# Kernel tuning notes

Measured on AMD Instinct MI355X. Metric: run time of the kernel, lower is better.

Reference implementation:

```python
import jax, jax.numpy as jnp
import numpy as np

N = 100000   # nodes
E = 1600000  # edges (avg degree 16)
F = 128      # num_features
H = 128      # hidden_channels
L = 3        # mp_layers
C = 40       # num_classes
EPS = 1e-5   # BatchNorm eps


def setup_inputs() -> dict:
    key = jax.random.key(0)
    ks = jax.random.split(key, 6)
    x = jax.random.normal(ks[0], (N, F), dtype=jnp.float32)
    edge_index = jax.random.randint(ks[1], (2, E), 0, N, dtype=jnp.int64)
    # GCNConv weights (F==H so all layers share shape), PyG-style lin + bias
    Ws = jax.random.normal(ks[2], (L, H, H), dtype=jnp.float32) * 0.05
    bs = jnp.zeros((L, H), dtype=jnp.float32)
    # BatchNorm affine params
    gammas = jnp.ones((L, H), dtype=jnp.float32)
    betas = jnp.zeros((L, H), dtype=jnp.float32)
    # output head: skip-concat dim = F + L*H
    W_out = jax.random.normal(ks[3], (F + L * H, C), dtype=jnp.float32) * 0.05
    b_out = jnp.zeros((C,), dtype=jnp.float32)
    return {"x": x, "Ws": Ws, "bs": bs, "gammas": gammas, "betas": betas,
            "W_out": W_out, "b_out": b_out, "edge_index": edge_index}


def reference(x, Ws, bs, gammas, betas, W_out, b_out, edge_index):
    src, dst = edge_index[0], edge_index[1]
    n = x.shape[0]
    # GCN symmetric normalization with self-loops (PyG gcn_norm, add_self_loops=True)
    deg = jax.ops.segment_sum(jnp.ones(src.shape[0], x.dtype), dst, num_segments=n) + 1.0
    dinv = jax.lax.rsqrt(deg)
    edge_norm = (dinv[src] * dinv[dst])[:, None]   # [E,1]
    self_norm = (dinv * dinv)[:, None]             # [N,1] self-loop contribution

    outs = [x]
    h = x
    for i in range(L):
        hw = h @ Ws[i]                                                   # [N,H]
        msg = hw[src] * edge_norm                                        # gather [E,H]
        agg = jax.ops.segment_sum(msg, dst, num_segments=n)              # scatter-add
        agg = agg + hw * self_norm + bs[i]
        # BatchNorm1d in training mode (batch stats, biased variance)
        mu = agg.mean(axis=0)
        var = agg.var(axis=0)
        h = gammas[i] * (agg - mu) * jax.lax.rsqrt(var + EPS) + betas[i]
        outs.append(h)  # dropout p=0.0 -> identity; skip=True collects each layer

    xcat = jnp.concatenate(outs, axis=1)  # [N, F + L*H]
    return xcat @ W_out + b_out
```

## Files before the change

kernel.cpp:

```cpp
#include <hip/hip_runtime.h>

#define NN 100000
#define NE 1600000
#define HD 128
#define NL 3
#define NC 40
#define NCP 48

#define NBK 196
#define NPB 512
#define BSH 9
#define CAP 9216
#define PCAP 13312
#define EPB 6400
#define NBINBLK 250

typedef unsigned int u32;
typedef unsigned short u16;
typedef __attribute__((ext_vector_type(8))) short short8;
typedef __attribute__((ext_vector_type(4))) float f32x4;

__device__ __forceinline__ float b2f(u16 h){
    union{u32 u; float f;} v; v.u = ((u32)h) << 16; return v.f;
}
__device__ __forceinline__ u16 f2b(float f){
    union{float f; u32 u;} v; v.f = f;
    u32 u = v.u;
    u32 r = (u + 0x7FFFu + ((u >> 16) & 1u)) >> 16;
    return (u16)r;
}

__global__ void k_conv_w(const float* __restrict__ Ws, u16* __restrict__ wt,
                         int* __restrict__ gcur, float* __restrict__ stats,
                         u16* __restrict__ hwzero, const float* __restrict__ Wout,
                         u16* __restrict__ woutt){
    int i = blockIdx.x * blockDim.x + threadIdx.x;
    if (i < NBK) gcur[i] = 0;
    if (i < NL * 2 * HD) stats[i] = 0.f;
    if (i < HD) hwzero[i] = 0;
    if (i < NL * NCP * HD){
        int l = i / (NCP * HD);
        int r = i % (NCP * HD);
        int n = r / HD;
        int k = r % HD;
        woutt[i] = (n < NC) ? f2b(Wout[(size_t)(HD + l * HD + k) * NC + n]) : (u16)0;
    }
    if (i >= NL * HD * HD) return;
    int l = i / (HD * HD);
    int r = i % (HD * HD);
    int n = r / HD;
    int k = r % HD;
    wt[i] = f2b(Ws[l * HD * HD + k * HD + n]);
}

__launch_bounds__(256)
__global__ void k_convhead(const float* __restrict__ x, const float* __restrict__ wout,
                           const float* __restrict__ bout, float* __restrict__ out,
                           u16* __restrict__ hA){
    __shared__ float wl[HD * NC];
    __shared__ float bl[NC];
    int tid = threadIdx.x;
    for (int i = tid; i < HD * NC; i += 256) wl[i] = wout[i];
    if (tid < NC) bl[tid] = bout[tid];
    __syncthreads();
    int n = blockIdx.x * 256 + tid;
    if (n >= NN) return;
    f32x4 acc[10];
    #pragma unroll
    for (int q = 0; q < 10; q++) acc[q] = *reinterpret_cast<const f32x4*>(&bl[q * 4]);
    const float* xr = x + (size_t)n * HD;
    #pragma unroll
    for (int k8 = 0; k8 < HD / 8; k8++){
        float4 v0 = reinterpret_cast<const float4*>(xr)[k8 * 2];
        float4 v1 = reinterpret_cast<const float4*>(xr)[k8 * 2 + 1];
        float xs[8] = {v0.x, v0.y, v0.z, v0.w, v1.x, v1.y, v1.z, v1.w};
        uint4 ov;
        u16* po = (u16*)&ov;
        #pragma unroll
        for (int t = 0; t < 8; t++){
            int f = k8 * 8 + t;
            po[t] = f2b(xs[t]);
            const f32x4* wr = reinterpret_cast<const f32x4*>(&wl[f * NC]);
            #pragma unroll
            for (int q = 0; q < 10; q++) acc[q] += xs[t] * wr[q];
        }
        reinterpret_cast<uint4*>(hA + (size_t)n * HD)[k8] = ov;
    }
    float* orw = out + (size_t)n * NC;
    #pragma unroll
    for (int q = 0; q < 10; q++) reinterpret_cast<f32x4*>(orw)[q] = acc[q];
}

__launch_bounds__(256)
__global__ void k_bin(const int* __restrict__ src, const int* __restrict__ dst,
                      int* __restrict__ gcur, uint2* __restrict__ bb){
    __shared__ int hist[NBK];
    __shared__ int lbase[NBK];
    __shared__ int gbase[NBK];
    __shared__ int cur[NBK];
    __shared__ int wsum[4];
    __shared__ uint2 stage[EPB];
    int tid = threadIdx.x;
    int e0 = blockIdx.x * EPB;
    for (int i = tid; i < NBK; i += 256) hist[i] = 0;
    __syncthreads();
    for (int k = tid; k < EPB; k += 256){
        int d = dst[e0 + k];
        atomicAdd(&hist[d >> BSH], 1);
    }
    __syncthreads();
    {
        int v = (tid < NBK) ? hist[tid] : 0;
        int lane = tid & 63, w = tid >> 6;
        int incl = v;
        #pragma unroll
        for (int dlt = 1; dlt < 64; dlt <<= 1){
            int t = __shfl_up(incl, dlt);
            if (lane >= dlt) incl += t;
        }
        if (lane == 63) wsum[w] = incl;
        __syncthreads();
        if (tid == 0){
            int run = 0;
            #pragma unroll
            for (int j = 0; j < 4; j++){ int t = wsum[j]; wsum[j] = run; run += t; }
        }
        __syncthreads();
        int excl = wsum[w] + incl - v;
        if (tid < NBK){ lbase[tid] = excl; cur[tid] = excl; }
    }
    __syncthreads();
    if (tid < NBK) gbase[tid] = atomicAdd(&gcur[tid], hist[tid]);
    __syncthreads();
    for (int k = tid; k < EPB; k += 256){
        int s = src[e0 + k], d = dst[e0 + k];
        int pos = atomicAdd(&cur[d >> BSH], 1);
        stage[pos] = make_uint2((u32)s, (u32)d);
    }
    __syncthreads();
    for (int k = tid; k < EPB; k += 256){
        uint2 sd = stage[k];
        int b = (int)(sd.y >> BSH);
        int g = gbase[b] + (k - lbase[b]);
        if (g < CAP) bb[(size_t)b * CAP + g] = sd;
    }
}

__launch_bounds__(512)
__global__ void k_csr(const int* __restrict__ gcur, const uint2* __restrict__ bb,
                      int* __restrict__ csr_src, int* __restrict__ offs,
                      int* __restrict__ oend, float* __restrict__ dinv){
    __shared__ int hist[NPB];
    __shared__ int cur[NPB];
    __shared__ int wsum[8];
    __shared__ int totp_s;
    __shared__ int lcsr[PCAP];
    int tid = threadIdx.x;
    int b = blockIdx.x;
    int cnt_b = gcur[b]; if (cnt_b > CAP) cnt_b = CAP;
    const uint2* eb = bb + (size_t)b * CAP;
    hist[tid] = 0;
    __syncthreads();
    for (int k = tid; k < cnt_b; k += 512)
        atomicAdd(&hist[eb[k].y & (NPB - 1)], 1);
    __syncthreads();
    int cnt = hist[tid];
    int ps = (1 + cnt + 7) & ~7;
    int lane = tid & 63, w = tid >> 6;
    int incl = ps;
    #pragma unroll
    for (int dlt = 1; dlt < 64; dlt <<= 1){
        int t = __shfl_up(incl, dlt);
        if (lane >= dlt) incl += t;
    }
    if (lane == 63) wsum[w] = incl;
    __syncthreads();
    if (tid == 0){
        int run = 0;
        #pragma unroll
        for (int j = 0; j < 8; j++){ int t = wsum[j]; wsum[j] = run; run += t; }
        totp_s = run;
    }
    __syncthreads();
    int excl = wsum[w] + incl - ps;
    int n = b * NPB + tid;
    offs[n] = b * PCAP + excl;
    oend[n] = b * PCAP + excl + ps;
    if (n < NN) dinv[n] = rsqrtf((float)(cnt + 1));
    cur[tid] = excl + 1;
    int totp = totp_s;
    __syncthreads();
    for (int k = tid; k < totp; k += 512) lcsr[k] = NN;
    __syncthreads();
    lcsr[excl] = (n < NN) ? n : NN;
    __syncthreads();
    for (int k = tid; k < cnt_b; k += 512){
        uint2 sd = eb[k];
        int pos = atomicAdd(&cur[sd.y & (NPB - 1)], 1);
        lcsr[pos] = (int)sd.x;
    }
    __syncthreads();
    for (int k = tid; k < totp; k += 512)
        csr_src[b * PCAP + k] = lcsr[k];
}

__launch_bounds__(256)
__global__ void k_gemm(const u16* __restrict__ h, const u16* __restrict__ wt,
                       const float* __restrict__ dinv, u16* __restrict__ out){
    __shared__ u16 wlds[HD * HD];
    int tid = threadIdx.x;
    {
        const uint4* g = reinterpret_cast<const uint4*>(wt);
        #pragma unroll
        for (int i = 0; i < 8; i++){
            int lin16 = tid + 256 * i;
            uint4 v = g[lin16];
            int c = lin16 >> 4;
            int addr16 = lin16 ^ (c & 7);
            reinterpret_cast<uint4*>(wlds)[addr16] = v;
        }
    }
    __syncthreads();

    int wv = tid >> 6, lane = tid & 63;
    int row_base = blockIdx.x * 64 + wv * 16;
    int arow = row_base + (lane & 15);
    if (arow >= NN) arow = NN - 1;
    int koff = (lane >> 4) * 8;

    f32x4 acc[8];
    #pragma unroll
    for (int t = 0; t < 8; t++) acc[t] = (f32x4){0.f, 0.f, 0.f, 0.f};

    #pragma unroll
    for (int kk = 0; kk < 4; kk++){
        short8 a = *reinterpret_cast<const short8*>(h + arow * HD + kk * 32 + koff);
        #pragma unroll
        for (int ct = 0; ct < 8; ct++){
            int c = ct * 16 + (lane & 15);
            int addr16 = (c * 16 + kk * 4 + (koff >> 3)) ^ (c & 7);
            short8 b = *reinterpret_cast<const short8*>(wlds + addr16 * 8);
            acc[ct] = __builtin_amdgcn_mfma_f32_16x16x32_bf16(a, b, acc[ct], 0, 0, 0);
        }
    }

    int drow = row_base + (lane >> 4) * 4;
    int dcol = lane & 15;
    float dv[4];
    #pragma unroll
    for (int r = 0; r < 4; r++){
        int rr = drow + r;
        dv[r] = dinv[rr < NN ? rr : NN - 1];
    }
    #pragma unroll
    for (int ct = 0; ct < 8; ct++){
        #pragma unroll
        for (int r = 0; r < 4; r++){
            int rr = drow + r;
            if (rr < NN) out[rr * HD + ct * 16 + dcol] = f2b(acc[ct][r] * dv[r]);
        }
    }
}

template<bool DO_HW>
__launch_bounds__(256)
__global__ void k_gemmbn(const u16* __restrict__ agg, const float* __restrict__ bn,
                         const u16* __restrict__ wt, const u16* __restrict__ woutt,
                         const float* __restrict__ dinv, u16* __restrict__ hw,
                         float* __restrict__ out){
    __shared__ u16 wlds[HD * HD];
    __shared__ u16 wolds[NCP * HD];
    __shared__ float Al[HD];
    __shared__ float Cl[HD];
    int tid = threadIdx.x;
    if (DO_HW){
        const uint4* g = reinterpret_cast<const uint4*>(wt);
        #pragma unroll
        for (int i = 0; i < 8; i++){
            int lin16 = tid + 256 * i;
            uint4 v = g[lin16];
            int c = lin16 >> 4;
            int addr16 = lin16 ^ (c & 7);
            reinterpret_cast<uint4*>(wlds)[addr16] = v;
        }
    }
    {
        const uint4* g = reinterpret_cast<const uint4*>(woutt);
        #pragma unroll
        for (int i = 0; i < 3; i++){
            int lin16 = tid + 256 * i;
            uint4 v = g[lin16];
            int c = lin16 >> 4;
            int addr16 = lin16 ^ (c & 7);
            reinterpret_cast<uint4*>(wolds)[addr16] = v;
        }
    }
    if (tid < HD){ Al[tid] = bn[tid]; Cl[tid] = bn[HD + tid]; }
    __syncthreads();

    int wv = tid >> 6, lane = tid & 63;
    int row_base = blockIdx.x * 64 + wv * 16;
    int arow = row_base + (lane & 15);
    if (arow >= NN) arow = NN - 1;
    int koff = (lane >> 4) * 8;

    f32x4 accW[8];
    f32x4 accH[3];
    #pragma unroll
    for (int t = 0; t < 8; t++) accW[t] = (f32x4){0.f, 0.f, 0.f, 0.f};
    #pragma unroll
    for (int t = 0; t < 3; t++) accH[t] = (f32x4){0.f, 0.f, 0.f, 0.f};

    #pragma unroll
    for (int kk = 0; kk < 4; kk++){
        int fb = kk * 32 + koff;
        short8 raw = *reinterpret_cast<const short8*>(agg + (size_t)arow * HD + fb);
        f32x4 A0 = *reinterpret_cast<const f32x4*>(&Al[fb]);
        f32x4 A1 = *reinterpret_cast<const f32x4*>(&Al[fb + 4]);
        f32x4 C0 = *reinterpret_cast<const f32x4*>(&Cl[fb]);
        f32x4 C1 = *reinterpret_cast<const f32x4*>(&Cl[fb + 4]);
        short8 a;
        #pragma unroll
        for (int j = 0; j < 4; j++){
            a[j]     = (short)f2b(b2f((u16)raw[j])     * A0[j] + C0[j]);
            a[j + 4] = (short)f2b(b2f((u16)raw[j + 4]) * A1[j] + C1[j]);
        }
        if (DO_HW){
            #pragma unroll
            for (int ct = 0; ct < 8; ct++){
                int c = ct * 16 + (lane & 15);
                int addr16 = (c * 16 + kk * 4 + (koff >> 3)) ^ (c & 7);
                short8 b = *reinterpret_cast<const short8*>(wlds + addr16 * 8);
                accW[ct] = __builtin_amdgcn_mfma_f32_16x16x32_bf16(a, b, accW[ct], 0, 0, 0);
            }
        }
        #pragma unroll
        for (int ht = 0; ht < 3; ht++){
            int c = ht * 16 + (lane & 15);
            int addr16 = (c * 16 + kk * 4 + (koff >> 3)) ^ (c & 7);
            short8 b = *reinterpret_cast<const short8*>(wolds + addr16 * 8);
            accH[ht] = __builtin_amdgcn_mfma_f32_16x16x32_bf16(a, b, accH[ht], 0, 0, 0);
        }
    }

    int drow = row_base + (lane >> 4) * 4;
    int dcol = lane & 15;
    if (DO_HW){
        float dv[4];
        #pragma unroll
        for (int r = 0; r < 4; r++){
            int rr = drow + r;
            dv[r] = dinv[rr < NN ? rr : NN - 1];
        }
        #pragma unroll
        for (int ct = 0; ct < 8; ct++){
            #pragma unroll
            for (int r = 0; r < 4; r++){
                int rr = drow + r;
                if (rr < NN) hw[rr * HD + ct * 16 + dcol] = f2b(accW[ct][r] * dv[r]);
            }
        }
    }
    #pragma unroll
    for (int ht = 0; ht < 3; ht++){
        int col = ht * 16 + dcol;
        if (col < NC){
            #pragma unroll
            for (int r = 0; r < 4; r++){
                int rr = drow + r;
                if (rr < NN) out[(size_t)rr * NC + col] += accH[ht][r];
            }
        }
    }
}

__launch_bounds__(256)
__global__ void k_agg(const u16* __restrict__ hw, const int* __restrict__ offs,
                      const int* __restrict__ oend, const int* __restrict__ csr_src,
                      const float* __restrict__ dinv, const float* __restrict__ bias,
                      u16* __restrict__ agg, float* __restrict__ sums){
    __shared__ float redS[4][HD];
    __shared__ float redQ[4][HD];
    int tid = threadIdx.x;
    int lane = tid & 63;
    int wv = tid >> 6;
    int f0 = lane * 2;
    float b0 = bias[f0], b1 = bias[f0 + 1];
    float s0 = 0.f, s1 = 0.f, q0 = 0.f, q1 = 0.f;
    int n0 = (blockIdx.x * 4 + wv) * 16;
    const u32* hw32 = reinterpret_cast<const u32*>(hw);

    for (int k = 0; k < 16; k++){
        int n = n0 + k;
        if (n >= NN) break;
        float a0 = 0.f, a1 = 0.f, c0 = 0.f, c1 = 0.f;
        int e = offs[n], e1 = oend[n];
        int rem = e1 - e;
        while (rem > 0){
            int win = rem < 64 ? rem : 64;
            int idxv = csr_src[e + lane];
            int nch = win >> 3;
            u32 va[8], vb[8];

            #pragma unroll
            for (int j = 0; j < 8; j++){
                u32 uid = (u32)__builtin_amdgcn_readlane(idxv, j);
                va[j] = hw32[(size_t)(uid << 6) + (u32)lane];
            }
            for (int c = 1; c < nch; c++){
                if (c & 1){
                    #pragma unroll
                    for (int j = 0; j < 8; j++){
                        u32 uid = (u32)__builtin_amdgcn_readlane(idxv, c * 8 + j);
                        vb[j] = hw32[(size_t)(uid << 6) + (u32)lane];
                    }
                    #pragma unroll
                    for (int j = 0; j < 8; j++){
                        union{u32 u; float f;} L, H;
                        L.u = va[j] << 16; H.u = va[j] & 0xFFFF0000u;
                        a0 += L.f; a1 += H.f;
                    }
                } else {
                    #pragma unroll
                    for (int j = 0; j < 8; j++){
                        u32 uid = (u32)__builtin_amdgcn_readlane(idxv, c * 8 + j);
                        va[j] = hw32[(size_t)(uid << 6) + (u32)lane];
                    }
                    #pragma unroll
                    for (int j = 0; j < 8; j++){
                        union{u32 u; float f;} L, H;
                        L.u = vb[j] << 16; H.u = vb[j] & 0xFFFF0000u;
                        c0 += L.f; c1 += H.f;
                    }
                }
            }
            if (nch & 1){
                #pragma unroll
                for (int j = 0; j < 8; j++){
                    union{u32 u; float f;} L, H;
                    L.u = va[j] << 16; H.u = va[j] & 0xFFFF0000u;
                    a0 += L.f; a1 += H.f;
                }
            } else {
                #pragma unroll
                for (int j = 0; j < 8; j++){
                    union{u32 u; float f;} L, H;
                    L.u = vb[j] << 16; H.u = vb[j] & 0xFFFF0000u;
                    c0 += L.f; c1 += H.f;
                }
            }
            e += win; rem -= win;
        }
        float di = dinv[n];
        a0 = (a0 + c0) * di + b0;
        a1 = (a1 + c1) * di + b1;
        u32 o = ((u32)f2b(a1) << 16) | (u32)f2b(a0);
        *reinterpret_cast<u32*>(agg + (size_t)n * HD + f0) = o;
        s0 += a0; s1 += a1; q0 += a0 * a0; q1 += a1 * a1;
    }

    redS[wv][f0] = s0; redS[wv][f0 + 1] = s1;
    redQ[wv][f0] = q0; redQ[wv][f0 + 1] = q1;
    __syncthreads();
    if (tid < HD){
        float ts = redS[0][tid] + redS[1][tid] + redS[2][tid] + redS[3][tid];
        float tq = redQ[0][tid] + redQ[1][tid] + redQ[2][tid] + redQ[3][tid];
        atomicAdd(&sums[tid], ts);
        atomicAdd(&sums[HD + tid], tq);
    }
}

__global__ void k_bnprep(const float* __restrict__ sums, const float* __restrict__ gamma,
                         const float* __restrict__ beta, float* __restrict__ bn){
    int f = threadIdx.x;
    if (f >= HD) return;
    float mu = sums[f] / (float)NN;
    float var = sums[HD + f] / (float)NN - mu * mu;
    float inv = rsqrtf(var + 1e-5f);
    float a = gamma[f] * inv;
    bn[f] = a;
    bn[HD + f] = beta[f] - mu * a;
}

extern "C" void kernel_launch(void* const* d_in, const int* in_sizes, int n_in,
                              void* d_out, int out_size, void* d_ws, size_t ws_size,
                              hipStream_t stream){
    const float* x      = (const float*)d_in[0];
    const float* Ws     = (const float*)d_in[1];
    const float* bs     = (const float*)d_in[2];
    const float* gammas = (const float*)d_in[3];
    const float* betas  = (const float*)d_in[4];
    const float* W_out  = (const float*)d_in[5];
    const float* b_out  = (const float*)d_in[6];
    const int*   ei     = (const int*)d_in[7];
    const int* src = ei;
    const int* dst = ei + NE;
    float* out = (float*)d_out;

    char* ws = (char*)d_ws;
    size_t off = 0;
    auto alloc = [&](size_t bytes) -> char* {
        char* p = ws + off;
        off += (bytes + 255) & ~(size_t)255;
        return p;
    };
    u16*   hA       = (u16*)alloc((size_t)NN * HD * 2);
    u16*   hw       = (u16*)alloc((size_t)(NN + 1) * HD * 2);
    u16*   aggb     = (u16*)alloc((size_t)NN * HD * 2);
    u16*   wt       = (u16*)alloc((size_t)NL * HD * HD * 2);
    u16*   woutt    = (u16*)alloc((size_t)NL * NCP * HD * 2);
    float* dinv     = (float*)alloc((size_t)NN * 4);
    int*   offs     = (int*)alloc((size_t)(NBK * NPB) * 4);
    int*   oend     = (int*)alloc((size_t)(NBK * NPB) * 4);
    int*   gcur     = (int*)alloc((size_t)NBK * 4);
    int*   csr_src  = (int*)alloc(((size_t)NBK * PCAP + 256) * 4);
    float* stats    = (float*)alloc((size_t)NL * 2 * HD * 4);
    float* bn       = (float*)alloc((size_t)2 * HD * 4);

    uint2* bb = (uint2*)aggb;

    k_conv_w<<<(NL * HD * HD + 255) / 256, 256, 0, stream>>>(Ws, wt, gcur, stats,
                                                             hw + (size_t)NN * HD,
                                                             W_out, woutt);
    k_bin<<<NBINBLK, 256, 0, stream>>>(src, dst, gcur, bb);
    k_csr<<<NBK, 512, 0, stream>>>(gcur, bb, csr_src, offs, oend, dinv);

    k_convhead<<<(NN + 255) / 256, 256, 0, stream>>>(x, W_out, b_out, out, hA);

    k_gemm<<<(NN + 63) / 64, 256, 0, stream>>>(hA, wt, dinv, hw);

    for (int l = 0; l < NL; l++){
        k_agg<<<(NN + 63) / 64, 256, 0, stream>>>(hw, offs, oend, csr_src, dinv,
                                                  bs + (size_t)l * HD, aggb,
                                                  stats + (size_t)l * 2 * HD);
        k_bnprep<<<1, 128, 0, stream>>>(stats + (size_t)l * 2 * HD,
                                        gammas + (size_t)l * HD, betas + (size_t)l * HD, bn);
        if (l < NL - 1){
            k_gemmbn<true><<<(NN + 63) / 64, 256, 0, stream>>>(
                aggb, bn, wt + (size_t)(l + 1) * HD * HD,
                woutt + (size_t)l * NCP * HD, dinv, hw, out);
        } else {
            k_gemmbn<false><<<(NN + 63) / 64, 256, 0, stream>>>(
                aggb, bn, nullptr, woutt + (size_t)l * NCP * HD, dinv, nullptr, out);
        }
    }
}
```

Before: 459.7 us.

## Fuse input conversion and head GEMM into first MFMA GEMM, inline BN prep, pack edges

Replaces the separate fp32 head kernel and bf16 conversion pass with a single kernel that converts x to bf16 on the fly. It computes both the first-layer GEMM and the x-part of the output head with MFMA, removing the intermediate hA buffer write and read. BatchNorm coefficient preparation moves into each gemmbn block, eliminating three tiny launches. Edge binning packs source and local destination into one 32-bit word, halving the bin buffer traffic. The head's x contribution is now computed from bf16 inputs instead of fp32, which lowers precision slightly.

```diff
diff --git a/kernel.cpp b/kernel.cpp
--- a/kernel.cpp
+++ b/kernel.cpp
@@ -38,12 +38,12 @@
     if (i < NBK) gcur[i] = 0;
     if (i < NL * 2 * HD) stats[i] = 0.f;
     if (i < HD) hwzero[i] = 0;
-    if (i < NL * NCP * HD){
-        int l = i / (NCP * HD);
+    if (i < (NL + 1) * NCP * HD){
+        int li = i / (NCP * HD);
         int r = i % (NCP * HD);
         int n = r / HD;
         int k = r % HD;
-        woutt[i] = (n < NC) ? f2b(Wout[(size_t)(HD + l * HD + k) * NC + n]) : (u16)0;
+        woutt[i] = (n < NC) ? f2b(Wout[(size_t)(li * HD + k) * NC + n]) : (u16)0;
     }
     if (i >= NL * HD * HD) return;
     int l = i / (HD * HD);
@@ -54,46 +54,8 @@
 }
 
 __launch_bounds__(256)
-__global__ void k_convhead(const float* __restrict__ x, const float* __restrict__ wout,
-                           const float* __restrict__ bout, float* __restrict__ out,
-                           u16* __restrict__ hA){
-    __shared__ float wl[HD * NC];
-    __shared__ float bl[NC];
-    int tid = threadIdx.x;
-    for (int i = tid; i < HD * NC; i += 256) wl[i] = wout[i];
-    if (tid < NC) bl[tid] = bout[tid];
-    __syncthreads();
-    int n = blockIdx.x * 256 + tid;
-    if (n >= NN) return;
-    f32x4 acc[10];
-    #pragma unroll
-    for (int q = 0; q < 10; q++) acc[q] = *reinterpret_cast<const f32x4*>(&bl[q * 4]);
-    const float* xr = x + (size_t)n * HD;
-    #pragma unroll
-    for (int k8 = 0; k8 < HD / 8; k8++){
-        float4 v0 = reinterpret_cast<const float4*>(xr)[k8 * 2];
-        float4 v1 = reinterpret_cast<const float4*>(xr)[k8 * 2 + 1];
-        float xs[8] = {v0.x, v0.y, v0.z, v0.w, v1.x, v1.y, v1.z, v1.w};
-        uint4 ov;
-        u16* po = (u16*)&ov;
-        #pragma unroll
-        for (int t = 0; t < 8; t++){
-            int f = k8 * 8 + t;
-            po[t] = f2b(xs[t]);
-            const f32x4* wr = reinterpret_cast<const f32x4*>(&wl[f * NC]);
-            #pragma unroll
-            for (int q = 0; q < 10; q++) acc[q] += xs[t] * wr[q];
-        }
-        reinterpret_cast<uint4*>(hA + (size_t)n * HD)[k8] = ov;
-    }
-    float* orw = out + (size_t)n * NC;
-    #pragma unroll
-    for (int q = 0; q < 10; q++) reinterpret_cast<f32x4*>(orw)[q] = acc[q];
-}
-
-__launch_bounds__(256)
 __global__ void k_bin(const int* __restrict__ src, const int* __restrict__ dst,
-                      int* __restrict__ gcur, uint2* __restrict__ bb){
+                      int* __restrict__ gcur, u32* __restrict__ bb){
     __shared__ int hist[NBK];
     __shared__ int lbase[NBK];
     __shared__ int gbase[NBK];
@@ -142,12 +104,12 @@
         uint2 sd = stage[k];
         int b = (int)(sd.y >> BSH);
         int g = gbase[b] + (k - lbase[b]);
-        if (g < CAP) bb[(size_t)b * CAP + g] = sd;
+        if (g < CAP) bb[(size_t)b * CAP + g] = sd.x | ((sd.y & (NPB - 1)) << 17);
     }
 }
 
 __launch_bounds__(512)
-__global__ void k_csr(const int* __restrict__ gcur, const uint2* __restrict__ bb,
+__global__ void k_csr(const int* __restrict__ gcur, const u32* __restrict__ bb,
                       int* __restrict__ csr_src, int* __restrict__ offs,
                       int* __restrict__ oend, float* __restrict__ dinv){
     __shared__ int hist[NPB];
@@ -158,11 +120,11 @@
     int tid = threadIdx.x;
     int b = blockIdx.x;
     int cnt_b = gcur[b]; if (cnt_b > CAP) cnt_b = CAP;
-    const uint2* eb = bb + (size_t)b * CAP;
+    const u32* eb = bb + (size_t)b * CAP;
     hist[tid] = 0;
     __syncthreads();
     for (int k = tid; k < cnt_b; k += 512)
-        atomicAdd(&hist[eb[k].y & (NPB - 1)], 1);
+        atomicAdd(&hist[eb[k] >> 17], 1);
     __syncthreads();
     int cnt = hist[tid];
     int ps = (1 + cnt + 7) & ~7;
@@ -195,9 +157,9 @@
     lcsr[excl] = (n < NN) ? n : NN;
     __syncthreads();
     for (int k = tid; k < cnt_b; k += 512){
-        uint2 sd = eb[k];
-        int pos = atomicAdd(&cur[sd.y & (NPB - 1)], 1);
-        lcsr[pos] = (int)sd.x;
+        u32 sd = eb[k];
+        int pos = atomicAdd(&cur[sd >> 17], 1);
+        lcsr[pos] = (int)(sd & 0x1FFFFu);
     }
     __syncthreads();
     for (int k = tid; k < totp; k += 512)
@@ -205,9 +167,13 @@
 }
 
 __launch_bounds__(256)
-__global__ void k_gemm(const u16* __restrict__ h, const u16* __restrict__ wt,
-                       const float* __restrict__ dinv, u16* __restrict__ out){
+__global__ void k_convgemm(const float* __restrict__ x, const u16* __restrict__ wt,
+                           const u16* __restrict__ woutt, const float* __restrict__ bout,
+                           const float* __restrict__ dinv, u16* __restrict__ hw,
+                           float* __restrict__ out){
     __shared__ u16 wlds[HD * HD];
+    __shared__ u16 wolds[NCP * HD];
+    __shared__ float bl[NC];
     int tid = threadIdx.x;
     {
         const uint4* g = reinterpret_cast<const uint4*>(wt);
@@ -220,6 +186,18 @@
             reinterpret_cast<uint4*>(wlds)[addr16] = v;
         }
     }
+    {
+        const uint4* g = reinterpret_cast<const uint4*>(woutt);
+        #pragma unroll
+        for (int i = 0; i < 3; i++){
+            int lin16 = tid + 256 * i;
+            uint4 v = g[lin16];
+            int c = lin16 >> 4;
+            int addr16 = lin16 ^ (c & 7);
+            reinterpret_cast<uint4*>(wolds)[addr16] = v;
+        }
+    }
+    if (tid < NC) bl[tid] = bout[tid];
     __syncthreads();
 
     int wv = tid >> 6, lane = tid & 63;
@@ -228,19 +206,37 @@
     if (arow >= NN) arow = NN - 1;
     int koff = (lane >> 4) * 8;
 
-    f32x4 acc[8];
-    #pragma unroll
-    for (int t = 0; t < 8; t++) acc[t] = (f32x4){0.f, 0.f, 0.f, 0.f};
+    f32x4 accW[8];
+    f32x4 accH[3];
+    #pragma unroll
+    for (int t = 0; t < 8; t++) accW[t] = (f32x4){0.f, 0.f, 0.f, 0.f};
+    #pragma unroll
+    for (int t = 0; t < 3; t++) accH[t] = (f32x4){0.f, 0.f, 0.f, 0.f};
 
     #pragma unroll
     for (int kk = 0; kk < 4; kk++){
-        short8 a = *reinterpret_cast<const short8*>(h + arow * HD + kk * 32 + koff);
+        int fb = kk * 32 + koff;
+        const float4* xr = reinterpret_cast<const float4*>(x + (size_t)arow * HD + fb);
+        float4 v0 = xr[0];
+        float4 v1 = xr[1];
+        short8 a;
+        a[0] = (short)f2b(v0.x); a[1] = (short)f2b(v0.y);
+        a[2] = (short)f2b(v0.z); a[3] = (short)f2b(v0.w);
+        a[4] = (short)f2b(v1.x); a[5] = (short)f2b(v1.y);
+        a[6] = (short)f2b(v1.z); a[7] = (short)f2b(v1.w);
         #pragma unroll
         for (int ct = 0; ct < 8; ct++){
             int c = ct * 16 + (lane & 15);
             int addr16 = (c * 16 + kk * 4 + (koff >> 3)) ^ (c & 7);
             short8 b = *reinterpret_cast<const short8*>(wlds + addr16 * 8);
-            acc[ct] = __builtin_amdgcn_mfma_f32_16x16x32_bf16(a, b, acc[ct], 0, 0, 0);
+            accW[ct] = __builtin_amdgcn_mfma_f32_16x16x32_bf16(a, b, accW[ct], 0, 0, 0);
+        }
+        #pragma unroll
+        for (int ht = 0; ht < 3; ht++){
+            int c = ht * 16 + (lane & 15);
+            int addr16 = (c * 16 + kk * 4 + (koff >> 3)) ^ (c & 7);
+            short8 b = *reinterpret_cast<const short8*>(wolds + addr16 * 8);
+            accH[ht] = __builtin_amdgcn_mfma_f32_16x16x32_bf16(a, b, accH[ht], 0, 0, 0);
         }
     }
 
@@ -257,14 +253,27 @@
         #pragma unroll
         for (int r = 0; r < 4; r++){
             int rr = drow + r;
-            if (rr < NN) out[rr * HD + ct * 16 + dcol] = f2b(acc[ct][r] * dv[r]);
+            if (rr < NN) hw[rr * HD + ct * 16 + dcol] = f2b(accW[ct][r] * dv[r]);
+        }
+    }
+    #pragma unroll
+    for (int ht = 0; ht < 3; ht++){
+        int col = ht * 16 + dcol;
+        if (col < NC){
+            float bv = bl[col];
+            #pragma unroll
+            for (int r = 0; r < 4; r++){
+                int rr = drow + r;
+                if (rr < NN) out[(size_t)rr * NC + col] = bv + accH[ht][r];
+            }
         }
     }
 }
 
 template<bool DO_HW>
 __launch_bounds__(256)
-__global__ void k_gemmbn(const u16* __restrict__ agg, const float* __restrict__ bn,
+__global__ void k_gemmbn(const u16* __restrict__ agg, const float* __restrict__ sums,
+                         const float* __restrict__ gamma, const float* __restrict__ beta,
                          const u16* __restrict__ wt, const u16* __restrict__ woutt,
                          const float* __restrict__ dinv, u16* __restrict__ hw,
                          float* __restrict__ out){
@@ -295,7 +304,14 @@
             reinterpret_cast<uint4*>(wolds)[addr16] = v;
         }
     }
-    if (tid < HD){ Al[tid] = bn[tid]; Cl[tid] = bn[HD + tid]; }
+    if (tid < HD){
+        float mu = sums[tid] / (float)NN;
+        float var = sums[HD + tid] / (float)NN - mu * mu;
+        float inv = rsqrtf(var + 1e-5f);
+        float a = gamma[tid] * inv;
+        Al[tid] = a;
+        Cl[tid] = beta[tid] - mu * a;
+    }
     __syncthreads();
 
     int wv = tid >> 6, lane = tid & 63;
@@ -470,18 +486,6 @@
     }
 }
 
-__global__ void k_bnprep(const float* __restrict__ sums, const float* __restrict__ gamma,
-                         const float* __restrict__ beta, float* __restrict__ bn){
-    int f = threadIdx.x;
-    if (f >= HD) return;
-    float mu = sums[f] / (float)NN;
-    float var = sums[HD + f] / (float)NN - mu * mu;
-    float inv = rsqrtf(var + 1e-5f);
-    float a = gamma[f] * inv;
-    bn[f] = a;
-    bn[HD + f] = beta[f] - mu * a;
-}
-
 extern "C" void kernel_launch(void* const* d_in, const int* in_sizes, int n_in,
                               void* d_out, int out_size, void* d_ws, size_t ws_size,
                               hipStream_t stream){
@@ -504,20 +508,18 @@
         off += (bytes + 255) & ~(size_t)255;
         return p;
     };
-    u16*   hA       = (u16*)alloc((size_t)NN * HD * 2);
     u16*   hw       = (u16*)alloc((size_t)(NN + 1) * HD * 2);
     u16*   aggb     = (u16*)alloc((size_t)NN * HD * 2);
     u16*   wt       = (u16*)alloc((size_t)NL * HD * HD * 2);
-    u16*   woutt    = (u16*)alloc((size_t)NL * NCP * HD * 2);
+    u16*   woutt    = (u16*)alloc((size_t)(NL + 1) * NCP * HD * 2);
     float* dinv     = (float*)alloc((size_t)NN * 4);
     int*   offs     = (int*)alloc((size_t)(NBK * NPB) * 4);
     int*   oend     = (int*)alloc((size_t)(NBK * NPB) * 4);
     int*   gcur     = (int*)alloc((size_t)NBK * 4);
     int*   csr_src  = (int*)alloc(((size_t)NBK * PCAP + 256) * 4);
     float* stats    = (float*)alloc((size_t)NL * 2 * HD * 4);
-    float* bn       = (float*)alloc((size_t)2 * HD * 4);
-
-    uint2* bb = (uint2*)aggb;
+
+    u32* bb = (u32*)aggb;
 
     k_conv_w<<<(NL * HD * HD + 255) / 256, 256, 0, stream>>>(Ws, wt, gcur, stats,
                                                              hw + (size_t)NN * HD,
@@ -525,23 +527,22 @@
     k_bin<<<NBINBLK, 256, 0, stream>>>(src, dst, gcur, bb);
     k_csr<<<NBK, 512, 0, stream>>>(gcur, bb, csr_src, offs, oend, dinv);
 
-    k_convhead<<<(NN + 255) / 256, 256, 0, stream>>>(x, W_out, b_out, out, hA);
-
-    k_gemm<<<(NN + 63) / 64, 256, 0, stream>>>(hA, wt, dinv, hw);
+    k_convgemm<<<(NN + 63) / 64, 256, 0, stream>>>(x, wt, woutt, b_out, dinv, hw, out);
 
     for (int l = 0; l < NL; l++){
         k_agg<<<(NN + 63) / 64, 256, 0, stream>>>(hw, offs, oend, csr_src, dinv,
                                                   bs + (size_t)l * HD, aggb,
                                                   stats + (size_t)l * 2 * HD);
-        k_bnprep<<<1, 128, 0, stream>>>(stats + (size_t)l * 2 * HD,
-                                        gammas + (size_t)l * HD, betas + (size_t)l * HD, bn);
         if (l < NL - 1){
             k_gemmbn<true><<<(NN + 63) / 64, 256, 0, stream>>>(
-                aggb, bn, wt + (size_t)(l + 1) * HD * HD,
-                woutt + (size_t)l * NCP * HD, dinv, hw, out);
+                aggb, stats + (size_t)l * 2 * HD, gammas + (size_t)l * HD,
+                betas + (size_t)l * HD, wt + (size_t)(l + 1) * HD * HD,
+                woutt + (size_t)(l + 1) * NCP * HD, dinv, hw, out);
         } else {
             k_gemmbn<false><<<(NN + 63) / 64, 256, 0, stream>>>(
-                aggb, bn, nullptr, woutt + (size_t)l * NCP * HD, dinv, nullptr, out);
-        }
-    }
-}
+                aggb, stats + (size_t)l * 2 * HD, gammas + (size_t)l * HD,
+                betas + (size_t)l * HD, nullptr,
+                woutt + (size_t)(l + 1) * NCP * HD, dinv, nullptr, out);
+        }
+    }
+}
```

After: 420.6 us. 8.5% less time.
